# Optimization experiments

Measured on AMD Instinct MI355X. Metric: run time of the kernel, lower is better.

## Reference

```python
import jax, jax.numpy as jnp
import numpy as np

LN_EPS = 1e-5
N_NODES = 100000
N_EDGES = 600000
HIDDEN = 128


def setup_inputs() -> dict:
    key = jax.random.key(0)
    ks = jax.random.split(key, 6)
    s = 1.0 / np.sqrt(HIDDEN)
    x = jax.random.normal(ks[0], (N_NODES, HIDDEN), dtype=jnp.float32)
    edge_index = jax.random.randint(ks[1], (2, N_EDGES), 0, N_NODES, dtype=jnp.int64)
    W1 = jax.random.normal(ks[2], (HIDDEN, HIDDEN), dtype=jnp.float32) * s
    b1 = jnp.zeros((HIDDEN,), dtype=jnp.float32)
    W2 = jax.random.normal(ks[3], (HIDDEN, HIDDEN), dtype=jnp.float32) * s
    b2 = jnp.zeros((HIDDEN,), dtype=jnp.float32)
    gamma = jnp.ones((HIDDEN,), dtype=jnp.float32)
    beta = jnp.zeros((HIDDEN,), dtype=jnp.float32)
    return {"x": x, "edge_index": edge_index, "W1": W1, "b1": b1,
            "W2": W2, "b2": b2, "gamma": gamma, "beta": beta}


def layer_norm(h, gamma, beta):
    mu = jnp.mean(h, axis=-1, keepdims=True)
    var = jnp.mean(jnp.square(h - mu), axis=-1, keepdims=True)
    return (h - mu) * jax.lax.rsqrt(var + LN_EPS) * gamma + beta


def reference(x, edge_index, W1, b1, W2, b2, gamma, beta):
    src, dst = edge_index[0], edge_index[1]
    # GIN aggregation (eps=0): (1+eps)*x + sum_{j in N(i)} x_j
    agg = x + jax.ops.segment_sum(x[src], dst, num_segments=x.shape[0])
    # MLP: Linear -> ReLU -> Linear
    h = jax.nn.relu(agg @ W1.T + b1) @ W2.T + b2
    h = jax.nn.relu(layer_norm(h, gamma, beta))
    # dropout is identity in eval mode
    return x + h
```

## Files before the change

### kernel.cpp

```cpp
#include <hip/hip_runtime.h>

#define H 128
#define LN_EPS 1e-5f
#define CAP 32

typedef __attribute__((ext_vector_type(8))) short bf16x8;
typedef __attribute__((ext_vector_type(4))) float f32x4;
typedef __attribute__((ext_vector_type(8))) unsigned short u16x8;

static __device__ __forceinline__ unsigned short f2bf(float f) {
  unsigned int u = __float_as_uint(f);
  u += 0x7fffu + ((u >> 16) & 1u);
  return (unsigned short)(u >> 16);
}

static __device__ __forceinline__ unsigned int cvt_pk_bf16(float lo, float hi) {
  unsigned int r;
  asm("v_cvt_pk_bf16_f32 %0, %1, %2" : "=v"(r) : "v"(lo), "v"(hi));
  return r;
}

static __device__ __forceinline__ void nt_st_f4(float* p, f32x4 v) {
  __builtin_nontemporal_store(v, (f32x4*)p);
}

static __device__ __forceinline__ void acc_bf8(float* a8, const uint4 v) {
  a8[0] += __uint_as_float(v.x << 16);
  a8[1] += __uint_as_float(v.x & 0xffff0000u);
  a8[2] += __uint_as_float(v.y << 16);
  a8[3] += __uint_as_float(v.y & 0xffff0000u);
  a8[4] += __uint_as_float(v.z << 16);
  a8[5] += __uint_as_float(v.z & 0xffff0000u);
  a8[6] += __uint_as_float(v.w << 16);
  a8[7] += __uint_as_float(v.w & 0xffff0000u);
}

template <int NT>
__device__ __forceinline__ void stage_w(const float* __restrict__ W,
                                        unsigned short* lds, int tid) {
#pragma unroll
  for (int it = 0; it < 4096 / NT; it++) {
    int i = tid + it * NT;
    int o = i >> 5;
    int k = (i & 31) << 2;
    float4 w = ((const float4*)W)[i];
    int byte = (o << 8) + (k << 1);
    byte ^= (o & 7) << 4;
    ushort4 wb;
    wb.x = f2bf(w.x); wb.y = f2bf(w.y); wb.z = f2bf(w.z); wb.w = f2bf(w.w);
    *(ushort4*)((char*)lds + byte) = wb;
  }
}

__global__ __launch_bounds__(256) void k_prep(
    const float* __restrict__ x, unsigned short* __restrict__ xb,
    const int* __restrict__ src, const int* __restrict__ dst,
    int* __restrict__ deg, int* __restrict__ slots, int ne, int nn) {
  const int t = blockIdx.x * 256 + threadIdx.x;
  const int nc = nn * 16;
  const bool do_cast = t < nc;
  const bool do_edge = t < ne;
  int d = 0, s = 0;
  if (do_edge) { d = dst[t]; s = src[t]; }
  float4 p, q;
  if (do_cast) {
    p = ((const float4*)x)[(size_t)t * 2];
    q = ((const float4*)x)[(size_t)t * 2 + 1];
  }
  if (do_cast) {
    u16x8 r;
    r[0] = f2bf(p.x); r[1] = f2bf(p.y); r[2] = f2bf(p.z); r[3] = f2bf(p.w);
    r[4] = f2bf(q.x); r[5] = f2bf(q.y); r[6] = f2bf(q.z); r[7] = f2bf(q.w);
    *(u16x8*)(xb + (size_t)t * 8) = r;
  }
  if (do_edge) {
    int pos = atomicAdd(&deg[d], 1);
    if (pos < CAP) slots[(size_t)pos * nn + d] = s;
  }
}

__global__ void k_fill_cm(const int* __restrict__ src, const int* __restrict__ dst,
                          int* __restrict__ deg, int* __restrict__ slots,
                          int ne, int nn) {
  int e = blockIdx.x * 256 + threadIdx.x;
  if (e >= ne) return;
  int d = dst[e];
  int p = atomicAdd(&deg[d], 1);
  if (p < CAP) slots[(size_t)p * nn + d] = src[e];
}

__global__ __launch_bounds__(512, 2) void k_mlp3b(
    const float* __restrict__ x, const unsigned short* __restrict__ xb,
    const int* __restrict__ deg, const int* __restrict__ slots,
    const float* __restrict__ W1, const float* __restrict__ b1,
    const float* __restrict__ W2, const float* __restrict__ b2,
    const float* __restrict__ gamma, const float* __restrict__ beta,
    float* __restrict__ out, int n_nodes) {
  __shared__ unsigned short Wlds[128 * 128];

  const int tid  = threadIdx.x;
  const int wave = tid >> 6;
  const int lane = tid & 63;
  const int l15  = lane & 15;
  const int lg   = lane >> 4;
  const int xorv = (l15 & 7) << 4;
  const int row_base = blockIdx.x * 128 + wave * 16;
  const bool active = row_base < n_nodes;

  stage_w<512>(W1, Wlds, tid);

  float a[4][8];
  float4 xres[8];
  if (active) {
    const int row = row_base + l15;
    const float* xr = x + (size_t)row * H + lg * 8;
#pragma unroll
    for (int ks = 0; ks < 4; ks++) {
      float4 p = *(const float4*)(xr + ks * 32);
      float4 q = *(const float4*)(xr + ks * 32 + 4);
      a[ks][0] = p.x; a[ks][1] = p.y; a[ks][2] = p.z; a[ks][3] = p.w;
      a[ks][4] = q.x; a[ks][5] = q.y; a[ks][6] = q.z; a[ks][7] = q.w;
    }
    const float* xrr = x + (size_t)row * H + lg * 4;
#pragma unroll
    for (int n = 0; n < 8; n++)
      xres[n] = *(const float4*)(xrr + n * 16);

    int d = deg[row];
    d = (d > CAP) ? CAP : d;
    const int* sl = slots + row;
    const int nn = n_nodes;
    const char* xbL = (const char*)xb + lg * 16;

    int s0 = (0 < d) ? sl[0] : 0;
    int s1 = (1 < d) ? sl[(size_t)1 * nn] : 0;
    int s2 = (2 < d) ? sl[(size_t)2 * nn] : 0;
    int s3 = (3 < d) ? sl[(size_t)3 * nn] : 0;
    uint4 va[4], vb[4];
    if (0 < d) {
      const char* pA = xbL + (size_t)s0 * 256;
#pragma unroll
      for (int ks = 0; ks < 4; ks++) va[ks] = *(const uint4*)(pA + ks * 64);
    }
    if (1 < d) {
      const char* pB = xbL + (size_t)s1 * 256;
#pragma unroll
      for (int ks = 0; ks < 4; ks++) vb[ks] = *(const uint4*)(pB + ks * 64);
    }
    int i = 0;
    for (; i + 2 <= d; i += 2) {
      uint4 na[4], nb[4];
      if (i + 2 < d) {
        const char* pA = xbL + (size_t)s2 * 256;
#pragma unroll
        for (int ks = 0; ks < 4; ks++) na[ks] = *(const uint4*)(pA + ks * 64);
      }
      if (i + 3 < d) {
        const char* pB = xbL + (size_t)s3 * 256;
#pragma unroll
        for (int ks = 0; ks < 4; ks++) nb[ks] = *(const uint4*)(pB + ks * 64);
      }
      const int ns2 = (i + 4 < d) ? sl[(size_t)(i + 4) * nn] : 0;
      const int ns3 = (i + 5 < d) ? sl[(size_t)(i + 5) * nn] : 0;
#pragma unroll
      for (int ks = 0; ks < 4; ks++) acc_bf8(a[ks], va[ks]);
      if (i + 1 < d) {
#pragma unroll
        for (int ks = 0; ks < 4; ks++) acc_bf8(a[ks], vb[ks]);
      }
#pragma unroll
      for (int ks = 0; ks < 4; ks++) { va[ks] = na[ks]; vb[ks] = nb[ks]; }
      s2 = ns2; s3 = ns3;
    }
    if (i < d) {
#pragma unroll
      for (int ks = 0; ks < 4; ks++) acc_bf8(a[ks], va[ks]);
    }
  }
  __syncthreads();

  unsigned int w0[8], w1[8];
  if (active) {
    bf16x8 af[4];
#pragma unroll
    for (int ks = 0; ks < 4; ks++)
#pragma unroll
      for (int j = 0; j < 8; j++) af[ks][j] = (short)f2bf(a[ks][j]);

    f32x4 acc1[8];
#pragma unroll
    for (int n = 0; n < 8; n++) acc1[n] = (f32x4){0.f, 0.f, 0.f, 0.f};
#pragma unroll
    for (int ks = 0; ks < 4; ks++) {
      const int k0 = ks * 32 + lg * 8;
#pragma unroll
      for (int n = 0; n < 8; n++) {
        const int o = n * 16 + l15;
        bf16x8 bf = *(const bf16x8*)((const char*)Wlds +
                     ((((o << 8) + (k0 << 1))) ^ xorv));
        acc1[n] = __builtin_amdgcn_mfma_f32_16x16x32_bf16(bf, af[ks], acc1[n], 0, 0, 0);
      }
    }
#pragma unroll
    for (int n = 0; n < 8; n++) {
      const float4 bb = *(const float4*)(b1 + n * 16 + lg * 4);
      float v0 = fmaxf(acc1[n][0] + bb.x, 0.f);
      float v1 = fmaxf(acc1[n][1] + bb.y, 0.f);
      float v2 = fmaxf(acc1[n][2] + bb.z, 0.f);
      float v3 = fmaxf(acc1[n][3] + bb.w, 0.f);
      w0[n] = cvt_pk_bf16(v0, v1);
      w1[n] = cvt_pk_bf16(v2, v3);
    }
  }
  __syncthreads();

  stage_w<512>(W2, Wlds, tid);

  bf16x8 a2f[4];
  if (active) {
    const int src_lo = ((lg & 1) << 5) + l15;
    const int src_hi = src_lo + 16;
    const bool nhi = (lg & 2) != 0;
#pragma unroll
    for (int ks = 0; ks < 4; ks++) {
      unsigned int m0a = __shfl(w0[2 * ks],     src_lo);
      unsigned int m0b = __shfl(w0[2 * ks + 1], src_lo);
      unsigned int m1a = __shfl(w1[2 * ks],     src_lo);
      unsigned int m1b = __shfl(w1[2 * ks + 1], src_lo);
      unsigned int m2a = __shfl(w0[2 * ks],     src_hi);
      unsigned int m2b = __shfl(w0[2 * ks + 1], src_hi);
      unsigned int m3a = __shfl(w1[2 * ks],     src_hi);
      unsigned int m3b = __shfl(w1[2 * ks + 1], src_hi);
      union { unsigned int u[4]; bf16x8 v; } c;
      c.u[0] = nhi ? m0b : m0a;
      c.u[1] = nhi ? m1b : m1a;
      c.u[2] = nhi ? m2b : m2a;
      c.u[3] = nhi ? m3b : m3a;
      a2f[ks] = c.v;
    }
  }
  __syncthreads();

  if (!active) return;

  f32x4 acc2[8];
#pragma unroll
  for (int n = 0; n < 8; n++) acc2[n] = (f32x4){0.f, 0.f, 0.f, 0.f};
#pragma unroll
  for (int ks = 0; ks < 4; ks++) {
    const int k0 = ks * 32 + lg * 8;
#pragma unroll
    for (int n = 0; n < 8; n++) {
      const int o = n * 16 + l15;
      bf16x8 bf = *(const bf16x8*)((const char*)Wlds +
                   ((((o << 8) + (k0 << 1))) ^ xorv));
      acc2[n] = __builtin_amdgcn_mfma_f32_16x16x32_bf16(bf, a2f[ks], acc2[n], 0, 0, 0);
    }
  }

  const int row = row_base + l15;
  float sum = 0.f, ssq = 0.f;
#pragma unroll
  for (int n = 0; n < 8; n++) {
    const float4 bb = *(const float4*)(b2 + n * 16 + lg * 4);
    acc2[n][0] += bb.x; acc2[n][1] += bb.y;
    acc2[n][2] += bb.z; acc2[n][3] += bb.w;
#pragma unroll
    for (int r = 0; r < 4; r++) {
      float v = acc2[n][r];
      sum += v;
      ssq += v * v;
    }
  }
  sum += __shfl_xor(sum, 16, 64);
  sum += __shfl_xor(sum, 32, 64);
  ssq += __shfl_xor(ssq, 16, 64);
  ssq += __shfl_xor(ssq, 32, 64);
  const float mu = sum * (1.0f / H);
  const float var = ssq * (1.0f / H) - mu * mu;
  const float rs = rsqrtf(var + LN_EPS);

#pragma unroll
  for (int n = 0; n < 8; n++) {
    const int col = n * 16 + lg * 4;
    const float4 g4  = *(const float4*)(gamma + col);
    const float4 be4 = *(const float4*)(beta + col);
    const float4 x4  = xres[n];
    f32x4 o4;
    o4.x = x4.x + fmaxf((acc2[n][0] - mu) * rs * g4.x + be4.x, 0.f);
    o4.y = x4.y + fmaxf((acc2[n][1] - mu) * rs * g4.y + be4.y, 0.f);
    o4.z = x4.z + fmaxf((acc2[n][2] - mu) * rs * g4.z + be4.z, 0.f);
    o4.w = x4.w + fmaxf((acc2[n][3] - mu) * rs * g4.w + be4.w, 0.f);
    nt_st_f4(out + (size_t)row * H + col, o4);
  }
}

__global__ __launch_bounds__(512, 4) void k_mlp3f(
    const float* __restrict__ x,
    const int* __restrict__ deg, const int* __restrict__ slots,
    const float* __restrict__ W1, const float* __restrict__ b1,
    const float* __restrict__ W2, const float* __restrict__ b2,
    const float* __restrict__ gamma, const float* __restrict__ beta,
    float* __restrict__ out, int n_nodes) {
  __shared__ unsigned short Wlds[128 * 128];

  const int tid  = threadIdx.x;
  const int wave = tid >> 6;
  const int lane = tid & 63;
  const int l15  = lane & 15;
  const int lg   = lane >> 4;
  const int xorv = (l15 & 7) << 4;
  const int row_base = blockIdx.x * 128 + wave * 16;
  const bool active = row_base < n_nodes;

  stage_w<512>(W1, Wlds, tid);

  float a[4][8];
  if (active) {
    const int row = row_base + l15;
    const float* xr = x + (size_t)row * H + lg * 8;
#pragma unroll
    for (int ks = 0; ks < 4; ks++) {
      float4 p = *(const float4*)(xr + ks * 32);
      float4 q = *(const float4*)(xr + ks * 32 + 4);
      a[ks][0] = p.x; a[ks][1] = p.y; a[ks][2] = p.z; a[ks][3] = p.w;
      a[ks][4] = q.x; a[ks][5] = q.y; a[ks][6] = q.z; a[ks][7] = q.w;
    }
    int d = deg[row];
    d = (d > CAP) ? CAP : d;
    const int* sl = slots + row;
    const int nn = n_nodes;

    int sA = (0 < d) ? sl[0] : 0;
    int sB = (1 < d) ? sl[(size_t)1 * nn] : 0;
    int i = 0;
    for (; i + 2 <= d; i += 2) {
      const int sA2 = (i + 2 < d) ? sl[(size_t)(i + 2) * nn] : 0;
      const int sB2 = (i + 3 < d) ? sl[(size_t)(i + 3) * nn] : 0;
      const float* xA = x + (size_t)sA * H + lg * 8;
      const float* xB = x + (size_t)sB * H + lg * 8;
      float4 pa[4], qa[4], pb[4], qb[4];
#pragma unroll
      for (int ks = 0; ks < 4; ks++) {
        pa[ks] = *(const float4*)(xA + ks * 32);
        qa[ks] = *(const float4*)(xA + ks * 32 + 4);
        pb[ks] = *(const float4*)(xB + ks * 32);
        qb[ks] = *(const float4*)(xB + ks * 32 + 4);
      }
#pragma unroll
      for (int ks = 0; ks < 4; ks++) {
        a[ks][0] += pa[ks].x + pb[ks].x;
        a[ks][1] += pa[ks].y + pb[ks].y;
        a[ks][2] += pa[ks].z + pb[ks].z;
        a[ks][3] += pa[ks].w + pb[ks].w;
        a[ks][4] += qa[ks].x + qb[ks].x;
        a[ks][5] += qa[ks].y + qb[ks].y;
        a[ks][6] += qa[ks].z + qb[ks].z;
        a[ks][7] += qa[ks].w + qb[ks].w;
      }
      sA = sA2; sB = sB2;
    }
    if (i < d) {
      const float* xA = x + (size_t)sA * H + lg * 8;
#pragma unroll
      for (int ks = 0; ks < 4; ks++) {
        float4 p = *(const float4*)(xA + ks * 32);
        float4 q = *(const float4*)(xA + ks * 32 + 4);
        a[ks][0] += p.x; a[ks][1] += p.y; a[ks][2] += p.z; a[ks][3] += p.w;
        a[ks][4] += q.x; a[ks][5] += q.y; a[ks][6] += q.z; a[ks][7] += q.w;
      }
    }
  }
  __syncthreads();

  unsigned int w0[8], w1[8];
  if (active) {
    bf16x8 af[4];
#pragma unroll
    for (int ks = 0; ks < 4; ks++)
#pragma unroll
      for (int j = 0; j < 8; j++) af[ks][j] = (short)f2bf(a[ks][j]);

    f32x4 acc1[8];
#pragma unroll
    for (int n = 0; n < 8; n++) acc1[n] = (f32x4){0.f, 0.f, 0.f, 0.f};
#pragma unroll
    for (int ks = 0; ks < 4; ks++) {
      const int k0 = ks * 32 + lg * 8;
#pragma unroll
      for (int n = 0; n < 8; n++) {
        const int o = n * 16 + l15;
        bf16x8 bf = *(const bf16x8*)((const char*)Wlds +
                     ((((o << 8) + (k0 << 1))) ^ xorv));
        acc1[n] = __builtin_amdgcn_mfma_f32_16x16x32_bf16(bf, af[ks], acc1[n], 0, 0, 0);
      }
    }
#pragma unroll
    for (int n = 0; n < 8; n++) {
      const float4 bb = *(const float4*)(b1 + n * 16 + lg * 4);
      float v0 = fmaxf(acc1[n][0] + bb.x, 0.f);
      float v1 = fmaxf(acc1[n][1] + bb.y, 0.f);
      float v2 = fmaxf(acc1[n][2] + bb.z, 0.f);
      float v3 = fmaxf(acc1[n][3] + bb.w, 0.f);
      w0[n] = cvt_pk_bf16(v0, v1);
      w1[n] = cvt_pk_bf16(v2, v3);
    }
  }
  __syncthreads();

  stage_w<512>(W2, Wlds, tid);

  bf16x8 a2f[4];
  if (active) {
    const int src_lo = ((lg & 1) << 5) + l15;
    const int src_hi = src_lo + 16;
    const bool nhi = (lg & 2) != 0;
#pragma unroll
    for (int ks = 0; ks < 4; ks++) {
      unsigned int m0a = __shfl(w0[2 * ks],     src_lo);
      unsigned int m0b = __shfl(w0[2 * ks + 1], src_lo);
      unsigned int m1a = __shfl(w1[2 * ks],     src_lo);
      unsigned int m1b = __shfl(w1[2 * ks + 1], src_lo);
      unsigned int m2a = __shfl(w0[2 * ks],     src_hi);
      unsigned int m2b = __shfl(w0[2 * ks + 1], src_hi);
      unsigned int m3a = __shfl(w1[2 * ks],     src_hi);
      unsigned int m3b = __shfl(w1[2 * ks + 1], src_hi);
      union { unsigned int u[4]; bf16x8 v; } c;
      c.u[0] = nhi ? m0b : m0a;
      c.u[1] = nhi ? m1b : m1a;
      c.u[2] = nhi ? m2b : m2a;
      c.u[3] = nhi ? m3b : m3a;
      a2f[ks] = c.v;
    }
  }
  __syncthreads();

  if (!active) return;

  f32x4 acc2[8];
#pragma unroll
  for (int n = 0; n < 8; n++) acc2[n] = (f32x4){0.f, 0.f, 0.f, 0.f};
#pragma unroll
  for (int ks = 0; ks < 4; ks++) {
    const int k0 = ks * 32 + lg * 8;
#pragma unroll
    for (int n = 0; n < 8; n++) {
      const int o = n * 16 + l15;
      bf16x8 bf = *(const bf16x8*)((const char*)Wlds +
                   ((((o << 8) + (k0 << 1))) ^ xorv));
      acc2[n] = __builtin_amdgcn_mfma_f32_16x16x32_bf16(bf, a2f[ks], acc2[n], 0, 0, 0);
    }
  }

  const int row = row_base + l15;
  float sum = 0.f, ssq = 0.f;
#pragma unroll
  for (int n = 0; n < 8; n++) {
    const float4 bb = *(const float4*)(b2 + n * 16 + lg * 4);
    acc2[n][0] += bb.x; acc2[n][1] += bb.y;
    acc2[n][2] += bb.z; acc2[n][3] += bb.w;
#pragma unroll
    for (int r = 0; r < 4; r++) {
      float v = acc2[n][r];
      sum += v;
      ssq += v * v;
    }
  }
  sum += __shfl_xor(sum, 16, 64);
  sum += __shfl_xor(sum, 32, 64);
  ssq += __shfl_xor(ssq, 16, 64);
  ssq += __shfl_xor(ssq, 32, 64);
  const float mu = sum * (1.0f / H);
  const float var = ssq * (1.0f / H) - mu * mu;
  const float rs = rsqrtf(var + LN_EPS);

#pragma unroll
  for (int n = 0; n < 8; n++) {
    const int col = n * 16 + lg * 4;
    const float4 g4  = *(const float4*)(gamma + col);
    const float4 be4 = *(const float4*)(beta + col);
    const float4 x4  = *(const float4*)(x + (size_t)row * H + col);
    float4 o4;
    o4.x = x4.x + fmaxf((acc2[n][0] - mu) * rs * g4.x + be4.x, 0.f);
    o4.y = x4.y + fmaxf((acc2[n][1] - mu) * rs * g4.y + be4.y, 0.f);
    o4.z = x4.z + fmaxf((acc2[n][2] - mu) * rs * g4.z + be4.z, 0.f);
    o4.w = x4.w + fmaxf((acc2[n][3] - mu) * rs * g4.w + be4.w, 0.f);
    *(float4*)(out + (size_t)row * H + col) = o4;
  }
}

extern "C" void kernel_launch(void* const* d_in, const int* in_sizes, int n_in,
                              void* d_out, int out_size, void* d_ws, size_t ws_size,
                              hipStream_t stream) {
  const float* x  = (const float*)d_in[0];
  const int*   ei = (const int*)d_in[1];
  const float* W1 = (const float*)d_in[2];
  const float* b1 = (const float*)d_in[3];
  const float* W2 = (const float*)d_in[4];
  const float* b2 = (const float*)d_in[5];
  const float* gm = (const float*)d_in[6];
  const float* bt = (const float*)d_in[7];
  float* out = (float*)d_out;

  const int n_nodes = in_sizes[0] / H;
  const int n_edges = in_sizes[1] / 2;
  const int* src = ei;
  const int* dst = ei + n_edges;

  const size_t slots_off = ((size_t)n_nodes + 63) & ~(size_t)63;
  const size_t xb_off    = slots_off + (size_t)CAP * n_nodes;
  const size_t need_bf   = (xb_off + (size_t)n_nodes * 64) * sizeof(int);
  const size_t need_cm   = xb_off * sizeof(int);

  if (ws_size >= need_bf) {
    int* deg   = (int*)d_ws;
    int* slots = (int*)d_ws + slots_off;
    unsigned short* xb = (unsigned short*)((int*)d_ws + xb_off);

    hipMemsetAsync(deg, 0, (size_t)n_nodes * sizeof(int), stream);
    const int ncast = n_nodes * 16;
    const int work = (n_edges > ncast) ? n_edges : ncast;
    k_prep<<<(work + 255) / 256, 256, 0, stream>>>(
        x, xb, src, dst, deg, slots, n_edges, n_nodes);
    k_mlp3b<<<(n_nodes + 127) / 128, 512, 0, stream>>>(
        x, xb, deg, slots, W1, b1, W2, b2, gm, bt, out, n_nodes);
    return;
  }

  if (ws_size >= need_cm) {
    int* deg   = (int*)d_ws;
    int* slots = (int*)d_ws + slots_off;

    hipMemsetAsync(deg, 0, (size_t)n_nodes * sizeof(int), stream);
    k_fill_cm<<<(n_edges + 255) / 256, 256, 0, stream>>>(
        src, dst, deg, slots, n_edges, n_nodes);
    k_mlp3f<<<(n_nodes + 127) / 128, 512, 0, stream>>>(
        x, deg, slots, W1, b1, W2, b2, gm, bt, out, n_nodes);
    return;
  }
}
```

Before: 124.4 us.

## Switch neighbor slot table to row-major and simplify gather prefetch

Stores the per-destination neighbor slots row-major (node*CAP+pos) instead of column-major, so each node's neighbor indices sit contiguously. The bf16 gather loop drops its software-pipelined prefetch of the next two neighbor rows and loads the current pair directly, reducing register pressure. Launch bounds rise from 2 to 4 blocks per CU to allow more occupancy. The row-major layout makes a lane's index reads contiguous but leaves adjacent lanes' reads strided, so per-wave coalescing on the slot reads is lost, and the gather loses explicit latency hiding.

```diff
diff --git a/kernel.cpp b/kernel.cpp
--- a/kernel.cpp
+++ b/kernel.cpp
@@ -75,21 +75,20 @@
   }
   if (do_edge) {
     int pos = atomicAdd(&deg[d], 1);
-    if (pos < CAP) slots[(size_t)pos * nn + d] = s;
-  }
-}
-
-__global__ void k_fill_cm(const int* __restrict__ src, const int* __restrict__ dst,
-                          int* __restrict__ deg, int* __restrict__ slots,
-                          int ne, int nn) {
+    if (pos < CAP) slots[(size_t)d * CAP + pos] = s;
+  }
+}
+
+__global__ void k_fill_rm(const int* __restrict__ src, const int* __restrict__ dst,
+                          int* __restrict__ deg, int* __restrict__ slots, int ne) {
   int e = blockIdx.x * 256 + threadIdx.x;
   if (e >= ne) return;
   int d = dst[e];
   int p = atomicAdd(&deg[d], 1);
-  if (p < CAP) slots[(size_t)p * nn + d] = src[e];
-}
-
-__global__ __launch_bounds__(512, 2) void k_mlp3b(
+  if (p < CAP) slots[(size_t)d * CAP + p] = src[e];
+}
+
+__global__ __launch_bounds__(512, 4) void k_mlp3b(
     const float* __restrict__ x, const unsigned short* __restrict__ xb,
     const int* __restrict__ deg, const int* __restrict__ slots,
     const float* __restrict__ W1, const float* __restrict__ b1,
@@ -128,53 +127,37 @@
 
     int d = deg[row];
     d = (d > CAP) ? CAP : d;
-    const int* sl = slots + row;
-    const int nn = n_nodes;
+    const int* sl = slots + (size_t)row * CAP;
     const char* xbL = (const char*)xb + lg * 16;
 
-    int s0 = (0 < d) ? sl[0] : 0;
-    int s1 = (1 < d) ? sl[(size_t)1 * nn] : 0;
-    int s2 = (2 < d) ? sl[(size_t)2 * nn] : 0;
-    int s3 = (3 < d) ? sl[(size_t)3 * nn] : 0;
-    uint4 va[4], vb[4];
-    if (0 < d) {
-      const char* pA = xbL + (size_t)s0 * 256;
-#pragma unroll
-      for (int ks = 0; ks < 4; ks++) va[ks] = *(const uint4*)(pA + ks * 64);
-    }
-    if (1 < d) {
-      const char* pB = xbL + (size_t)s1 * 256;
-#pragma unroll
-      for (int ks = 0; ks < 4; ks++) vb[ks] = *(const uint4*)(pB + ks * 64);
-    }
+    int sA = (0 < d) ? sl[0] : 0;
+    int sB = (1 < d) ? sl[1] : 0;
     int i = 0;
     for (; i + 2 <= d; i += 2) {
-      uint4 na[4], nb[4];
-      if (i + 2 < d) {
-        const char* pA = xbL + (size_t)s2 * 256;
-#pragma unroll
-        for (int ks = 0; ks < 4; ks++) na[ks] = *(const uint4*)(pA + ks * 64);
-      }
-      if (i + 3 < d) {
-        const char* pB = xbL + (size_t)s3 * 256;
-#pragma unroll
-        for (int ks = 0; ks < 4; ks++) nb[ks] = *(const uint4*)(pB + ks * 64);
-      }
-      const int ns2 = (i + 4 < d) ? sl[(size_t)(i + 4) * nn] : 0;
-      const int ns3 = (i + 5 < d) ? sl[(size_t)(i + 5) * nn] : 0;
-#pragma unroll
-      for (int ks = 0; ks < 4; ks++) acc_bf8(a[ks], va[ks]);
-      if (i + 1 < d) {
-#pragma unroll
-        for (int ks = 0; ks < 4; ks++) acc_bf8(a[ks], vb[ks]);
-      }
-#pragma unroll
-      for (int ks = 0; ks < 4; ks++) { va[ks] = na[ks]; vb[ks] = nb[ks]; }
-      s2 = ns2; s3 = ns3;
+      const int sA2 = (i + 2 < d) ? sl[i + 2] : 0;
+      const int sB2 = (i + 3 < d) ? sl[i + 3] : 0;
+      const char* pA = xbL + (size_t)sA * 256;
+      const char* pB = xbL + (size_t)sB * 256;
+      uint4 va[4], vb[4];
+#pragma unroll
+      for (int ks = 0; ks < 4; ks++) {
+        va[ks] = *(const uint4*)(pA + ks * 64);
+        vb[ks] = *(const uint4*)(pB + ks * 64);
+      }
+#pragma unroll
+      for (int ks = 0; ks < 4; ks++) {
+        acc_bf8(a[ks], va[ks]);
+        acc_bf8(a[ks], vb[ks]);
+      }
+      sA = sA2; sB = sB2;
     }
     if (i < d) {
-#pragma unroll
-      for (int ks = 0; ks < 4; ks++) acc_bf8(a[ks], va[ks]);
+      const char* pA = xbL + (size_t)sA * 256;
+#pragma unroll
+      for (int ks = 0; ks < 4; ks++) {
+        uint4 v = *(const uint4*)(pA + ks * 64);
+        acc_bf8(a[ks], v);
+      }
     }
   }
   __syncthreads();
@@ -328,15 +311,14 @@
     }
     int d = deg[row];
     d = (d > CAP) ? CAP : d;
-    const int* sl = slots + row;
-    const int nn = n_nodes;
+    const int* sl = slots + (size_t)row * CAP;
 
     int sA = (0 < d) ? sl[0] : 0;
-    int sB = (1 < d) ? sl[(size_t)1 * nn] : 0;
+    int sB = (1 < d) ? sl[1] : 0;
     int i = 0;
     for (; i + 2 <= d; i += 2) {
-      const int sA2 = (i + 2 < d) ? sl[(size_t)(i + 2) * nn] : 0;
-      const int sB2 = (i + 3 < d) ? sl[(size_t)(i + 3) * nn] : 0;
+      const int sA2 = (i + 2 < d) ? sl[i + 2] : 0;
+      const int sB2 = (i + 3 < d) ? sl[i + 3] : 0;
       const float* xA = x + (size_t)sA * H + lg * 8;
       const float* xB = x + (size_t)sB * H + lg * 8;
       float4 pa[4], qa[4], pb[4], qb[4];
@@ -508,7 +490,7 @@
   const int* dst = ei + n_edges;
 
   const size_t slots_off = ((size_t)n_nodes + 63) & ~(size_t)63;
-  const size_t xb_off    = slots_off + (size_t)CAP * n_nodes;
+  const size_t xb_off    = slots_off + (size_t)n_nodes * CAP;
   const size_t need_bf   = (xb_off + (size_t)n_nodes * 64) * sizeof(int);
   const size_t need_cm   = xb_off * sizeof(int);
 
@@ -532,8 +514,8 @@
     int* slots = (int*)d_ws + slots_off;
 
     hipMemsetAsync(deg, 0, (size_t)n_nodes * sizeof(int), stream);
-    k_fill_cm<<<(n_edges + 255) / 256, 256, 0, stream>>>(
-        src, dst, deg, slots, n_edges, n_nodes);
+    k_fill_rm<<<(n_edges + 255) / 256, 256, 0, stream>>>(
+        src, dst, deg, slots, n_edges);
     k_mlp3f<<<(n_nodes + 127) / 128, 512, 0, stream>>>(
         x, deg, slots, W1, b1, W2, b2, gm, bt, out, n_nodes);
     return;
```

After: 143.3 us. 15.2% more time.
